# Optimization experiments

Measured on AMD Instinct MI355X. Metric: run time of the kernel, lower is better.

## Reference

```python
import jax, jax.numpy as jnp
import numpy as np

B, T, I, H, HORIZON = 64, 512, 256, 1024, 24


def _lstm_layer(x, Wih, Whh, bih, bhh):
    """PyTorch-convention LSTM layer. x: [B,T,I_l] -> outputs [B,T,H].
    Gate order along 4H axis: i, f, g, o."""
    b = x.shape[0]
    h_dim = Whh.shape[1]
    # Precompute input contribution for all timesteps: [B,T,4H]
    xg = jnp.einsum('bti,gi->btg', x, Wih) + bih + bhh

    def step(carry, xg_t):
        h, c = carry
        gates = xg_t + h @ Whh.T  # [B,4H]
        i_g, f_g, g_g, o_g = jnp.split(gates, 4, axis=-1)
        c = jax.nn.sigmoid(f_g) * c + jax.nn.sigmoid(i_g) * jnp.tanh(g_g)
        h = jax.nn.sigmoid(o_g) * jnp.tanh(c)
        return (h, c), h

    h0 = jnp.zeros((b, h_dim), x.dtype)
    (_, _), hs = jax.lax.scan(step, (h0, h0), jnp.swapaxes(xg, 0, 1))
    return jnp.swapaxes(hs, 0, 1)  # [B,T,H]


def setup_inputs() -> dict:
    key = jax.random.key(0)
    ks = jax.random.split(key, 11)
    s_i = 1.0 / np.sqrt(H)  # PyTorch-style uniform-ish scale, use scaled normal
    return {
        'x': jax.random.normal(ks[0], (B, T, I), jnp.float32),
        'W_ih0': jax.random.normal(ks[1], (4 * H, I), jnp.float32) * s_i,
        'W_hh0': jax.random.normal(ks[2], (4 * H, H), jnp.float32) * s_i,
        'b_ih0': jax.random.normal(ks[3], (4 * H,), jnp.float32) * s_i,
        'b_hh0': jax.random.normal(ks[4], (4 * H,), jnp.float32) * s_i,
        'W_ih1': jax.random.normal(ks[5], (4 * H, H), jnp.float32) * s_i,
        'W_hh1': jax.random.normal(ks[6], (4 * H, H), jnp.float32) * s_i,
        'b_ih1': jax.random.normal(ks[7], (4 * H,), jnp.float32) * s_i,
        'b_hh1': jax.random.normal(ks[8], (4 * H,), jnp.float32) * s_i,
        'W_head': jax.random.normal(ks[9], (HORIZON, H), jnp.float32) * s_i,
        'b_head': jax.random.normal(ks[10], (HORIZON,), jnp.float32) * s_i,
    }


def reference(x, W_ih0, W_hh0, b_ih0, b_hh0, W_ih1, W_hh1, b_ih1, b_hh1, W_head, b_head):
    h1 = _lstm_layer(x, W_ih0, W_hh0, b_ih0, b_hh0)   # [B,T,H]
    h2 = _lstm_layer(h1, W_ih1, W_hh1, b_ih1, b_hh1)  # [B,T,H]
    last = h2[:, -1, :]                                # [B,H]
    return last @ W_head.T + b_head                    # [B,HORIZON]
```

## Files before the change

kernel.cpp:

```cpp
#include <hip/hip_runtime.h>


typedef _Float16 h8 __attribute__((ext_vector_type(8)));
typedef float    f4 __attribute__((ext_vector_type(4)));
typedef unsigned long long u64;

#define WS_W0P   0
#define WS_W1P   10485760
#define WS_H0Q   27262976
#define WS_H2Q   27787264
#define WS_SYNC  28049408
#define WS_XPK   28057600
#define WS_XPK_END 44834816ULL

static __device__ __forceinline__ float sigm(float v) { return 1.f / (1.f + __expf(-v)); }
static __device__ __forceinline__ float tanh_fast(float v) {
  const float e = __expf(2.f * v);
  return 1.f - 2.f / (e + 1.f);
}
static __device__ __forceinline__ h8 vload16(const _Float16* p) {
  return *(const volatile h8*)p;
}
static __device__ __forceinline__ void vstore16(_Float16* p, h8 v) {
  *(volatile h8*)p = v;
}

__global__ void prep_kernel(const float* __restrict__ x,
                            const float* __restrict__ Wih0, const float* __restrict__ Whh0,
                            const float* __restrict__ Wih1, const float* __restrict__ Whh1,
                            _Float16* __restrict__ W0p, _Float16* __restrict__ W1p,
                            _Float16* __restrict__ xpk,
                            unsigned* __restrict__ hz, unsigned* __restrict__ sync_ws)
{
  const long tid0 = (long)blockIdx.x * blockDim.x + threadIdx.x;
  const long np   = (long)gridDim.x * blockDim.x;

  for (long e = tid0; e < 5242880; e += np) {
    const int j = e & 7, quad = (e >> 3) & 3, l15 = (e >> 5) & 15, nt = (e >> 9) & 7;
    const int r = (int)(e >> 12);
    const int c = r % 40, cs = r / 40;
    const int col = nt * 16 + l15;
    const int row = (col >> 5) * 1024 + cs * 32 + (col & 31);
    const int k = c * 32 + quad * 8 + j;
    const float v = (k < 256) ? Wih0[(long)row * 256 + k] : Whh0[(long)row * 1024 + k - 256];
    W0p[e] = (_Float16)v;
  }
  for (long e = tid0; e < 8388608; e += np) {
    const int j = e & 7, quad = (e >> 3) & 3, l15 = (e >> 5) & 15, nt = (e >> 9) & 7;
    const int r = (int)(e >> 12);
    const int c = r & 63, cs = r >> 6;
    const int col = nt * 16 + l15;
    const int row = (col >> 5) * 1024 + cs * 32 + (col & 31);
    const int k = c * 32 + quad * 8 + j;
    const float v = (k < 1024) ? Wih1[(long)row * 1024 + k] : Whh1[(long)row * 1024 + k - 1024];
    W1p[e] = (_Float16)v;
  }
  if (xpk) {
    for (long e = tid0; e < 8388608; e += np) {
      const int k32 = e & 31, b16 = (e >> 5) & 15, bg = (e >> 9) & 3;
      const int c = (e >> 11) & 7;
      const int t = (int)(e >> 14);
      const int b = bg * 16 + b16, k = c * 32 + k32;
      xpk[e] = (_Float16)x[(long)b * 131072 + (long)t * 256 + k];
    }
  }
  for (long e = tid0; e < 196608; e += np) hz[e] = 0u;
  if (tid0 < 2048) sync_ws[tid0] = 0u;
}

template<bool XP>
__launch_bounds__(512, 1)
__global__ void lstm_kernel(const float* __restrict__ x, const _Float16* __restrict__ xpk,
                            const float* __restrict__ bih0, const float* __restrict__ bhh0,
                            const float* __restrict__ bih1, const float* __restrict__ bhh1,
                            const _Float16* __restrict__ W0p, const _Float16* __restrict__ W1p,
                            _Float16* __restrict__ h0q, _Float16* __restrict__ h2q,
                            unsigned* __restrict__ sy)
{
  extern __shared__ float gb[];
  __shared__ float cst[512];
  __shared__ float biasl[128];
  __shared__ _Float16 htmp[32 * 18];

  const int tid = threadIdx.x, wg = blockIdx.x;
  const int xcd = wg & 7, jdec = wg >> 3;
  const int lay = jdec & 1, jj = jdec >> 1;
  const int bg = jj & 3, csl = jj >> 2;
  const int cs = xcd * 4 + csl;
  const int lane = tid & 63, kg = tid >> 6;
  const int l15 = lane & 15, quad = lane >> 4;
  const int boff = l15 * 32 + quad * 8;
  const int aoff = bg * 512 + l15 * 32 + quad * 8;

  const _Float16* Wp = lay ? (W1p + (long)cs * 262144) : (W0p + (long)cs * 163840);

  if (tid < 128) {
    const int row = (tid >> 5) * 1024 + cs * 32 + (tid & 31);
    biasl[tid] = lay ? (bih1[row] + bhh1[row]) : (bih0[row] + bhh0[row]);
  }
  cst[tid] = 0.f;
  __syncthreads();

  unsigned* const fL0  = sy + (bg * 32) * 8;
  unsigned* const fL1  = sy + ((4 + bg) * 32) * 8;
  unsigned* const fOwn = (lay ? fL1 : fL0) + cs * 8;

  auto spin = [&](const unsigned* p, int tgt) {
    if (tgt <= 0) return;
    while ((int)__hip_atomic_load(p, __ATOMIC_RELAXED, __HIP_MEMORY_SCOPE_AGENT) < tgt)
      __builtin_amdgcn_s_sleep(1);
  };

  auto dump = [&](const f4* acc) {
#pragma unroll
    for (int nt = 0; nt < 8; ++nt)
      *(f4*)&gb[(kg * 128 + nt * 16 + l15) * 24 + quad * 4] = acc[nt];
  };

  auto pointwise_publish = [&](_Float16* wr, int n) {
    __syncthreads();
    {
      const int b16 = tid & 15, hh = tid >> 4;
      float gv[4];
#pragma unroll
      for (int gt = 0; gt < 4; ++gt) {
        float s = biasl[gt * 32 + hh];
#pragma unroll
        for (int k = 0; k < 8; ++k) s += gb[(k * 128 + gt * 32 + hh) * 24 + b16];
        gv[gt] = s;
      }
      const float si = sigm(gv[0]), sf = sigm(gv[1]);
      const float tg = tanh_fast(gv[2]), so = sigm(gv[3]);
      const float cn = sf * cst[tid] + si * tg;
      cst[tid] = cn;
      htmp[hh * 18 + b16] = (_Float16)(so * tanh_fast(cn));
    }
    __syncthreads();
    if (tid < 64) {
      const int b16 = tid & 15, q = tid >> 4;
      union { h8 v; _Float16 e[8]; } r;
#pragma unroll
      for (int i = 0; i < 8; ++i) r.e[i] = htmp[(q * 8 + i) * 18 + b16];
      vstore16(wr + (cs * 4 + bg) * 512 + b16 * 32 + q * 8, r.v);
      asm volatile("s_waitcnt vmcnt(0)" ::: "memory");
      if (tid == 0)
        __hip_atomic_store(fOwn, (unsigned)(n + 1),
                           __ATOMIC_RELAXED, __HIP_MEMORY_SCOPE_AGENT);
    }
  };

  if (lay == 0) {
    const int c0 = kg * 5;
    for (int n = 0; n < 512; ++n) {
      const _Float16* h0prev = h0q + ((n - 1) & 3) * 65536;
      const _Float16* xs = XP ? (xpk + (long)n * 16384) : nullptr;

      f4 acc[8] = {};
      h8 Ab[5]; h8 Bb[2][8];
      auto loadB = [&](int c, int sl) {
        const _Float16* bp = Wp + (long)c * 4096 + boff;
#pragma unroll
        for (int nt = 0; nt < 8; ++nt) Bb[sl][nt] = *(const h8*)(bp + nt * 512);
      };
      auto loadA = [&](int c, int idx) {
        if (c < 8) {
          if (XP) Ab[idx] = *(const h8*)(xs + c * 2048 + aoff);
          else {
            const float* q = x + (long)(bg * 16 + l15) * 131072 + (long)n * 256 + c * 32 + quad * 8;
            const f4 v0 = *(const f4*)q;
            const f4 v1 = *(const f4*)(q + 4);
            h8 t;
            t[0]=(_Float16)v0[0]; t[1]=(_Float16)v0[1]; t[2]=(_Float16)v0[2]; t[3]=(_Float16)v0[3];
            t[4]=(_Float16)v1[0]; t[5]=(_Float16)v1[1]; t[6]=(_Float16)v1[2]; t[7]=(_Float16)v1[3];
            Ab[idx] = t;
          }
        } else {
          Ab[idx] = vload16(h0prev + (c - 8) * 2048 + aoff);
        }
      };

      loadB(c0, 0);
#pragma unroll
      for (int i = 0; i < 5; ++i)
        if (c0 + i < 8) loadA(c0 + i, i);

      if (kg == 1) {
        if (lane < 32) spin(fL0 + lane * 8, n);
        else           spin(fL1 + (lane - 32) * 8, n - 3);
      }
      __syncthreads();

#pragma unroll
      for (int i = 0; i < 5; ++i)
        if (c0 + i >= 8) loadA(c0 + i, i);

#pragma unroll
      for (int i = 0; i < 5; ++i) {
        if (i + 1 < 5) loadB(c0 + i + 1, (i + 1) & 1);
        const h8 A = Ab[i];
#pragma unroll
        for (int nt = 0; nt < 8; ++nt)
          acc[nt] = __builtin_amdgcn_mfma_f32_16x16x32_f16(A, Bb[i & 1][nt], acc[nt], 0, 0, 0);
      }
      dump(acc);
      pointwise_publish(h0q + (n & 3) * 65536, n);
    }
  } else {
    const int c0 = kg * 4;
    for (int n = 0; n < 512; ++n) {
      const _Float16* h0cur  = h0q + (n & 3) * 65536;
      const _Float16* h2prev = h2q + ((n - 1) & 1) * 65536;

      f4 acc[8] = {};
      h8 Ab[4]; h8 Bb[2][8];
      auto loadB = [&](int c, int sl) {
        const _Float16* bp = Wp + (long)c * 4096 + boff;
#pragma unroll
        for (int nt = 0; nt < 8; ++nt) Bb[sl][nt] = *(const h8*)(bp + nt * 512);
      };
      auto loadA = [&](const _Float16* hb, int cloc, int idx) {
        Ab[idx] = vload16(hb + cloc * 2048 + aoff);
      };

      loadB(32 + c0, 0);
      if (kg == 1) {
        if (lane < 32) spin(fL1 + lane * 8, n);
      }
      __syncthreads();
#pragma unroll
      for (int i = 0; i < 4; ++i) loadA(h2prev, c0 + i, i);
#pragma unroll
      for (int i = 0; i < 4; ++i) {
        if (i + 1 < 4) loadB(32 + c0 + i + 1, (i + 1) & 1);
        const h8 A = Ab[i];
#pragma unroll
        for (int nt = 0; nt < 8; ++nt)
          acc[nt] = __builtin_amdgcn_mfma_f32_16x16x32_f16(A, Bb[i & 1][nt], acc[nt], 0, 0, 0);
      }

      loadB(c0, 0);
      if (kg == 1) {
        if (lane < 32) spin(fL0 + lane * 8, n + 1);
      }
      __syncthreads();
#pragma unroll
      for (int i = 0; i < 4; ++i) loadA(h0cur, c0 + i, i);
#pragma unroll
      for (int i = 0; i < 4; ++i) {
        if (i + 1 < 4) loadB(c0 + i + 1, (i + 1) & 1);
        const h8 A = Ab[i];
#pragma unroll
        for (int nt = 0; nt < 8; ++nt)
          acc[nt] = __builtin_amdgcn_mfma_f32_16x16x32_f16(A, Bb[i & 1][nt], acc[nt], 0, 0, 0);
      }
      dump(acc);
      pointwise_publish(h2q + (n & 1) * 65536, n);
    }
  }
}

__global__ void head_kernel(const _Float16* __restrict__ h2s, const float* __restrict__ Wh,
                            const float* __restrict__ bh, float* __restrict__ out)
{
  const int blk = blockIdx.x;
  const int b = blk / 24, j = blk % 24;
  const int lane = threadIdx.x;
  float sum = 0.f;
#pragma unroll
  for (int k0 = 0; k0 < 1024; k0 += 64) {
    const int hid = k0 + lane;
    const float hv = (float)h2s[((hid >> 5) * 4 + (b >> 4)) * 512 + (b & 15) * 32 + (hid & 31)];
    sum += hv * Wh[(long)j * 1024 + hid];
  }
#pragma unroll
  for (int off = 32; off > 0; off >>= 1)
    sum += __shfl_down(sum, off, 64);
  if (lane == 0) out[b * 24 + j] = sum + bh[j];
}

extern "C" void kernel_launch(void* const* d_in, const int* in_sizes, int n_in,
                              void* d_out, int out_size, void* d_ws, size_t ws_size,
                              hipStream_t stream)
{
  const float* x    = (const float*)d_in[0];
  const float* Wih0 = (const float*)d_in[1];
  const float* Whh0 = (const float*)d_in[2];
  const float* bih0 = (const float*)d_in[3];
  const float* bhh0 = (const float*)d_in[4];
  const float* Wih1 = (const float*)d_in[5];
  const float* Whh1 = (const float*)d_in[6];
  const float* bih1 = (const float*)d_in[7];
  const float* bhh1 = (const float*)d_in[8];
  const float* Whd  = (const float*)d_in[9];
  const float* bhd  = (const float*)d_in[10];

  char* ws = (char*)d_ws;
  _Float16* W0p     = (_Float16*)(ws + WS_W0P);
  _Float16* W1p     = (_Float16*)(ws + WS_W1P);
  _Float16* h0q     = (_Float16*)(ws + WS_H0Q);
  _Float16* h2q     = (_Float16*)(ws + WS_H2Q);
  unsigned* sync_ws = (unsigned*)(ws + WS_SYNC);
  float* out = (float*)d_out;

  const bool use_xpk = (ws_size >= WS_XPK_END);
  _Float16* xpk = use_xpk ? (_Float16*)(ws + WS_XPK) : nullptr;

  prep_kernel<<<dim3(2048), dim3(256), 0, stream>>>(
      x, Wih0, Whh0, Wih1, Whh1, W0p, W1p, xpk,
      (unsigned*)(ws + WS_H0Q), sync_ws);

  if (use_xpk)
    lstm_kernel<true><<<dim3(256), dim3(512), 98304, stream>>>(
        x, xpk, bih0, bhh0, bih1, bhh1, W0p, W1p, h0q, h2q, sync_ws);
  else
    lstm_kernel<false><<<dim3(256), dim3(512), 98304, stream>>>(
        x, nullptr, bih0, bhh0, bih1, bhh1, W0p, W1p, h0q, h2q, sync_ws);

  head_kernel<<<dim3(64 * 24), dim3(64), 0, stream>>>(
      h2q + 65536, Whd, bhd, out);
}
```

Baseline: 5.114 ms.

## Replace block-wide flag spins with per-wave fine-grained waits and reorder layer-1 phases

```diff
diff --git a/kernel.cpp b/kernel.cpp
--- a/kernel.cpp
+++ b/kernel.cpp
@@ -101,14 +101,13 @@
   cst[tid] = 0.f;
   __syncthreads();
 
-  unsigned* const fL0  = sy + (bg * 32) * 8;
-  unsigned* const fL1  = sy + ((4 + bg) * 32) * 8;
-  unsigned* const fOwn = (lay ? fL1 : fL0) + cs * 8;
-
-  auto spin = [&](const unsigned* p, int tgt) {
-    if (tgt <= 0) return;
+  unsigned* const fL0  = sy + (bg * 32);
+  unsigned* const fL1  = sy + ((4 + bg) * 32);
+  unsigned* const fOwn = (lay ? fL1 : fL0) + cs;
+
+  auto spin1 = [&](const unsigned* p, int tgt) {
     while ((int)__hip_atomic_load(p, __ATOMIC_RELAXED, __HIP_MEMORY_SCOPE_AGENT) < tgt)
-      __builtin_amdgcn_s_sleep(1);
+      __builtin_amdgcn_s_sleep(2);
   };
 
   auto dump = [&](const f4* acc) {
@@ -117,7 +116,7 @@
       *(f4*)&gb[(kg * 128 + nt * 16 + l15) * 24 + quad * 4] = acc[nt];
   };
 
-  auto pointwise_publish = [&](_Float16* wr, int n) {
+  auto pointwise_publish = [&](_Float16* wr, int n, int gtgt) {
     __syncthreads();
     {
       const int b16 = tid & 15, hh = tid >> 4;
@@ -137,6 +136,7 @@
     }
     __syncthreads();
     if (tid < 64) {
+      if (tid < 32) spin1(fL1 + tid, gtgt);
       const int b16 = tid & 15, q = tid >> 4;
       union { h8 v; _Float16 e[8]; } r;
 #pragma unroll
@@ -184,11 +184,10 @@
       for (int i = 0; i < 5; ++i)
         if (c0 + i < 8) loadA(c0 + i, i);
 
-      if (kg == 1) {
-        if (lane < 32) spin(fL0 + lane * 8, n);
-        else           spin(fL1 + (lane - 32) * 8, n - 3);
-      }
-      __syncthreads();
+      if (lane < 5) {
+        const int c = c0 + lane;
+        if (c >= 8) spin1(fL0 + (c - 8), n);
+      }
 
 #pragma unroll
       for (int i = 0; i < 5; ++i)
@@ -203,7 +202,7 @@
           acc[nt] = __builtin_amdgcn_mfma_f32_16x16x32_f16(A, Bb[i & 1][nt], acc[nt], 0, 0, 0);
       }
       dump(acc);
-      pointwise_publish(h0q + (n & 3) * 65536, n);
+      pointwise_publish(h0q + (n & 3) * 65536, n, n - 3);
     }
   } else {
     const int c0 = kg * 4;
@@ -222,11 +221,21 @@
         Ab[idx] = vload16(hb + cloc * 2048 + aoff);
       };
 
+      loadB(c0, 0);
+      if (lane < 4) spin1(fL0 + c0 + lane, n + 1);
+#pragma unroll
+      for (int i = 0; i < 4; ++i) loadA(h0cur, c0 + i, i);
+#pragma unroll
+      for (int i = 0; i < 4; ++i) {
+        if (i + 1 < 4) loadB(c0 + i + 1, (i + 1) & 1);
+        const h8 A = Ab[i];
+#pragma unroll
+        for (int nt = 0; nt < 8; ++nt)
+          acc[nt] = __builtin_amdgcn_mfma_f32_16x16x32_f16(A, Bb[i & 1][nt], acc[nt], 0, 0, 0);
+      }
+
       loadB(32 + c0, 0);
-      if (kg == 1) {
-        if (lane < 32) spin(fL1 + lane * 8, n);
-      }
-      __syncthreads();
+      if (lane < 4) spin1(fL1 + c0 + lane, n);
 #pragma unroll
       for (int i = 0; i < 4; ++i) loadA(h2prev, c0 + i, i);
 #pragma unroll
@@ -237,24 +246,8 @@
         for (int nt = 0; nt < 8; ++nt)
           acc[nt] = __builtin_amdgcn_mfma_f32_16x16x32_f16(A, Bb[i & 1][nt], acc[nt], 0, 0, 0);
       }
-
-      loadB(c0, 0);
-      if (kg == 1) {
-        if (lane < 32) spin(fL0 + lane * 8, n + 1);
-      }
-      __syncthreads();
-#pragma unroll
-      for (int i = 0; i < 4; ++i) loadA(h0cur, c0 + i, i);
-#pragma unroll
-      for (int i = 0; i < 4; ++i) {
-        if (i + 1 < 4) loadB(c0 + i + 1, (i + 1) & 1);
-        const h8 A = Ab[i];
-#pragma unroll
-        for (int nt = 0; nt < 8; ++nt)
-          acc[nt] = __builtin_amdgcn_mfma_f32_16x16x32_f16(A, Bb[i & 1][nt], acc[nt], 0, 0, 0);
-      }
       dump(acc);
-      pointwise_publish(h2q + (n & 1) * 65536, n);
+      pointwise_publish(h2q + (n & 1) * 65536, n, n);
     }
   }
 }
```

Measured after the change: 4.564 ms. -10.8%, faster.
